# Performance work log

Measured on AMD Instinct MI355X. Metric: run time of the kernel, lower is better.

The kernel has to match this reference:

```python
import jax, jax.numpy as jnp
import numpy as np

B = 2097152
C = 10  # CIFAR-10 classes, hardcoded via `for j in range(10)` in the original


def setup_inputs() -> dict:
    key = jax.random.key(0)
    k1, k2, k3 = jax.random.split(key, 3)
    inp = jax.random.normal(k1, (B, C), dtype=jnp.float32)
    distance_matrix = jax.random.uniform(k2, (C, C), dtype=jnp.float32)
    target = jax.random.randint(k3, (B,), 0, C, dtype=jnp.int64)
    return {"input": inp, "distance_matrix": distance_matrix, "target": target}


def reference(input, distance_matrix, target):
    # distance_vector[i] = distance_matrix[target[i]]  -> [B, C]
    dv = distance_matrix[target]
    # distance_rank = argsort indices of each row (index of j-th smallest), as float
    r = jnp.argsort(dv, axis=1).astype(jnp.float32)  # [B, C]
    rt = jnp.take_along_axis(r, target[:, None], axis=1)  # [B, 1] rank entry at target position
    margins = jnp.maximum(0.0, 1.0 + r - rt)  # [B, C]
    mask = jnp.arange(C)[None, :] != target[:, None]  # exclude j == target[i]
    ranking_loss = jnp.sum(jnp.where(mask, margins, 0.0))
    # cross_entropy with mean reduction
    logp = jax.nn.log_softmax(input, axis=1)
    ce = -jnp.mean(jnp.take_along_axis(logp, target[:, None], axis=1))
    return ce + ranking_loss / input.shape[0]
```

## Files before the change

### kernel.cpp

```cpp
#include <hip/hip_runtime.h>

#define THREADS 256
#define BLOCKS  1024

__device__ __forceinline__ float row_loss10(
    float a0, float a1, float a2, float a3, float a4,
    float a5, float a6, float a7, float a8, float a9,
    int t, float sm)
{
    float m = fmaxf(fmaxf(fmaxf(a0, a1), fmaxf(a2, a3)),
                    fmaxf(fmaxf(fmaxf(a4, a5), fmaxf(a6, a7)), fmaxf(a8, a9)));
    float e0 = __expf(a0 - m), e1 = __expf(a1 - m);
    float e2 = __expf(a2 - m), e3 = __expf(a3 - m);
    float e4 = __expf(a4 - m), e5 = __expf(a5 - m);
    float e6 = __expf(a6 - m), e7 = __expf(a7 - m);
    float e8 = __expf(a8 - m), e9 = __expf(a9 - m);
    float s = ((e0 + e1) + (e2 + e3)) + (((e4 + e5) + (e6 + e7)) + (e8 + e9));
    float xt = a0;
    xt = (t == 1) ? a1 : xt;
    xt = (t == 2) ? a2 : xt;
    xt = (t == 3) ? a3 : xt;
    xt = (t == 4) ? a4 : xt;
    xt = (t == 5) ? a5 : xt;
    xt = (t == 6) ? a6 : xt;
    xt = (t == 7) ? a7 : xt;
    xt = (t == 8) ? a8 : xt;
    xt = (t == 9) ? a9 : xt;
    return m + __logf(s) - xt + sm;
}

__device__ __noinline__ float margin_for(const float* __restrict__ dm, int t) {
    float row[10];
    #pragma unroll
    for (int k = 0; k < 10; ++k) row[k] = dm[t * 10 + k];
    int rt = 0;
    #pragma unroll
    for (int k = 0; k < 10; ++k) {
        int cnt = 0;
        #pragma unroll
        for (int mi = 0; mi < 10; ++mi)
            cnt += (row[mi] < row[k]) || (row[mi] == row[k] && mi < k);
        if (cnt == t) rt = k;
    }
    float f = (float)(10 - rt);
    return 0.5f * f * (f + 1.0f) - 1.0f;
}

__global__ __launch_bounds__(THREADS, 4) void ranking_loss_kernel(
    const float* __restrict__ input,
    const float* __restrict__ dm,
    const int* __restrict__ target,
    float* __restrict__ partials,
    int B)
{
    __shared__ float4 stage[THREADS / 64][5 * 64];

    const int tid  = threadIdx.x;
    const int lane = tid & 63;
    const int wave = tid >> 6;

    float smval = 0.0f;
    if (lane < 10) {
        float row[10];
        #pragma unroll
        for (int k = 0; k < 10; ++k) row[k] = dm[lane * 10 + k];
        int rt = 0;
        #pragma unroll
        for (int k = 0; k < 10; ++k) {
            int cnt = 0;
            #pragma unroll
            for (int mi = 0; mi < 10; ++mi)
                cnt += (row[mi] < row[k]) || (row[mi] == row[k] && mi < k);
            if (cnt == lane) rt = k;
        }
        float f = (float)(10 - rt);
        smval = 0.5f * f * (f + 1.0f) - 1.0f;
    }

    const int nPairs  = B >> 1;
    const int gstride = gridDim.x * THREADS;
    float acc = 0.0f;

    float4* ws = stage[wave];
    int p0 = blockIdx.x * THREADS + wave * 64;

    float4 r0, r1, r2, r3, r4;
    int2 tt;
    bool have = (p0 + 64 <= nPairs);
    if (have) {
        const float4* g = (const float4*)input + (size_t)p0 * 5;
        r0 = g[0 * 64 + lane];
        r1 = g[1 * 64 + lane];
        r2 = g[2 * 64 + lane];
        r3 = g[3 * 64 + lane];
        r4 = g[4 * 64 + lane];
        tt = ((const int2*)target)[p0 + lane];
    }
    while (have) {
        ws[0 * 64 + lane] = r0;
        ws[1 * 64 + lane] = r1;
        ws[2 * 64 + lane] = r2;
        ws[3 * 64 + lane] = r3;
        ws[4 * 64 + lane] = r4;
        int2 ttc = tt;

        const int pn = p0 + gstride;
        const bool havenext = (pn + 64 <= nPairs);
        if (havenext) {
            const float4* g = (const float4*)input + (size_t)pn * 5;
            r0 = g[0 * 64 + lane];
            r1 = g[1 * 64 + lane];
            r2 = g[2 * 64 + lane];
            r3 = g[3 * 64 + lane];
            r4 = g[4 * 64 + lane];
            tt = ((const int2*)target)[pn + lane];
        }

        const float4* rp = &ws[(size_t)lane * 5];
        float4 q0 = rp[0], q1 = rp[1], q2 = rp[2], q3 = rp[3], q4 = rp[4];

        float sm0 = __shfl(smval, ttc.x, 64);
        float sm1 = __shfl(smval, ttc.y, 64);
        acc += row_loss10(q0.x, q0.y, q0.z, q0.w, q1.x, q1.y, q1.z, q1.w,
                          q2.x, q2.y, ttc.x, sm0);
        acc += row_loss10(q2.z, q2.w, q3.x, q3.y, q3.z, q3.w, q4.x, q4.y,
                          q4.z, q4.w, ttc.y, sm1);

        p0 = pn;
        have = havenext;
    }

    if (p0 < nPairs) {
        const int p = p0 + lane;
        if (p < nPairs) {
            const float* x = input + (size_t)p * 20;
            int t0 = target[2 * p], t1 = target[2 * p + 1];
            acc += row_loss10(x[0], x[1], x[2], x[3], x[4],
                              x[5], x[6], x[7], x[8], x[9], t0, margin_for(dm, t0));
            acc += row_loss10(x[10], x[11], x[12], x[13], x[14],
                              x[15], x[16], x[17], x[18], x[19], t1, margin_for(dm, t1));
        }
    }
    if ((B & 1) && blockIdx.x == 0 && tid == 0) {
        const float* x = input + (size_t)(B - 1) * 10;
        int t = target[B - 1];
        acc += row_loss10(x[0], x[1], x[2], x[3], x[4],
                          x[5], x[6], x[7], x[8], x[9], t, margin_for(dm, t));
    }

    #pragma unroll
    for (int off = 32; off > 0; off >>= 1)
        acc += __shfl_down(acc, off, 64);

    float* swsum = (float*)&stage[0][0];
    __syncthreads();
    if (lane == 0) swsum[wave] = acc;
    __syncthreads();
    if (tid == 0) {
        partials[blockIdx.x] = (swsum[0] + swsum[1]) + (swsum[2] + swsum[3]);
    }
}

__global__ __launch_bounds__(256) void reduce_kernel(
    const float* __restrict__ partials, float* __restrict__ out, float invB)
{
    __shared__ float sw[4];
    float a = 0.0f;
    #pragma unroll
    for (int k = 0; k < BLOCKS / 256; ++k)
        a += partials[k * 256 + threadIdx.x];
    #pragma unroll
    for (int off = 32; off > 0; off >>= 1)
        a += __shfl_down(a, off, 64);
    const int lane = threadIdx.x & 63;
    const int wave = threadIdx.x >> 6;
    if (lane == 0) sw[wave] = a;
    __syncthreads();
    if (threadIdx.x == 0)
        out[0] = ((sw[0] + sw[1]) + (sw[2] + sw[3])) * invB;
}

extern "C" void kernel_launch(void* const* d_in, const int* in_sizes, int n_in,
                              void* d_out, int out_size, void* d_ws, size_t ws_size,
                              hipStream_t stream) {
    const float* input  = (const float*)d_in[0];
    const float* dm     = (const float*)d_in[1];
    const int*   target = (const int*)d_in[2];
    float* out      = (float*)d_out;
    float* partials = (float*)d_ws;

    const int B = in_sizes[0] / 10;

    ranking_loss_kernel<<<BLOCKS, THREADS, 0, stream>>>(input, dm, target, partials, B);
    reduce_kernel<<<1, 256, 0, stream>>>(partials, out, 1.0f / (float)B);
}
```

Baseline: 131.3 us.

## Drop register prefetch, use nontemporal loads and double grid occupancy

Removes the software register double-buffering of the next tile, so each iteration loads, stages and computes in one step. Global loads become nontemporal, and the grid grows from 1024 to 2048 blocks while launch bounds rise to 8 waves per SIMD. The idea is to hide memory latency with more resident waves instead of per-thread prefetch registers. The risk is that without the explicit prefetch each wave stalls on its own loads, so the occupancy gain has to make up for that.

```diff
diff --git a/kernel.cpp b/kernel.cpp
--- a/kernel.cpp
+++ b/kernel.cpp
@@ -1,7 +1,10 @@
 #include <hip/hip_runtime.h>
 
 #define THREADS 256
-#define BLOCKS  1024
+#define BLOCKS  2048
+
+typedef float f4v __attribute__((ext_vector_type(4)));
+typedef int   i2v __attribute__((ext_vector_type(2)));
 
 __device__ __forceinline__ float row_loss10(
     float a0, float a1, float a2, float a3, float a4,
@@ -46,14 +49,14 @@
     return 0.5f * f * (f + 1.0f) - 1.0f;
 }
 
-__global__ __launch_bounds__(THREADS, 4) void ranking_loss_kernel(
+__global__ __launch_bounds__(THREADS, 8) void ranking_loss_kernel(
     const float* __restrict__ input,
     const float* __restrict__ dm,
     const int* __restrict__ target,
     float* __restrict__ partials,
     int B)
 {
-    __shared__ float4 stage[THREADS / 64][5 * 64];
+    __shared__ f4v stage[THREADS / 64][5 * 64];
 
     const int tid  = threadIdx.x;
     const int lane = tid & 63;
@@ -81,53 +84,33 @@
     const int gstride = gridDim.x * THREADS;
     float acc = 0.0f;
 
-    float4* ws = stage[wave];
+    f4v* ws = stage[wave];
     int p0 = blockIdx.x * THREADS + wave * 64;
 
-    float4 r0, r1, r2, r3, r4;
-    int2 tt;
-    bool have = (p0 + 64 <= nPairs);
-    if (have) {
-        const float4* g = (const float4*)input + (size_t)p0 * 5;
-        r0 = g[0 * 64 + lane];
-        r1 = g[1 * 64 + lane];
-        r2 = g[2 * 64 + lane];
-        r3 = g[3 * 64 + lane];
-        r4 = g[4 * 64 + lane];
-        tt = ((const int2*)target)[p0 + lane];
-    }
-    while (have) {
+    for (; p0 + 64 <= nPairs; p0 += gstride) {
+        const f4v* g = (const f4v*)input + (size_t)p0 * 5;
+        f4v r0 = __builtin_nontemporal_load(&g[0 * 64 + lane]);
+        f4v r1 = __builtin_nontemporal_load(&g[1 * 64 + lane]);
+        f4v r2 = __builtin_nontemporal_load(&g[2 * 64 + lane]);
+        f4v r3 = __builtin_nontemporal_load(&g[3 * 64 + lane]);
+        f4v r4 = __builtin_nontemporal_load(&g[4 * 64 + lane]);
+        i2v tt = __builtin_nontemporal_load(&((const i2v*)target)[p0 + lane]);
+
         ws[0 * 64 + lane] = r0;
         ws[1 * 64 + lane] = r1;
         ws[2 * 64 + lane] = r2;
         ws[3 * 64 + lane] = r3;
         ws[4 * 64 + lane] = r4;
-        int2 ttc = tt;
 
-        const int pn = p0 + gstride;
-        const bool havenext = (pn + 64 <= nPairs);
-        if (havenext) {
-            const float4* g = (const float4*)input + (size_t)pn * 5;
-            r0 = g[0 * 64 + lane];
-            r1 = g[1 * 64 + lane];
-            r2 = g[2 * 64 + lane];
-            r3 = g[3 * 64 + lane];
-            r4 = g[4 * 64 + lane];
-            tt = ((const int2*)target)[pn + lane];
-        }
+        const f4v* rp = &ws[(size_t)lane * 5];
+        f4v q0 = rp[0], q1 = rp[1], q2 = rp[2], q3 = rp[3], q4 = rp[4];
 
-        const float4* rp = &ws[(size_t)lane * 5];
-        float4 q0 = rp[0], q1 = rp[1], q2 = rp[2], q3 = rp[3], q4 = rp[4];
-
-        float sm0 = __shfl(smval, ttc.x, 64);
-        float sm1 = __shfl(smval, ttc.y, 64);
+        float sm0 = __shfl(smval, tt.x, 64);
+        float sm1 = __shfl(smval, tt.y, 64);
         acc += row_loss10(q0.x, q0.y, q0.z, q0.w, q1.x, q1.y, q1.z, q1.w,
-                          q2.x, q2.y, ttc.x, sm0);
+                          q2.x, q2.y, tt.x, sm0);
         acc += row_loss10(q2.z, q2.w, q3.x, q3.y, q3.z, q3.w, q4.x, q4.y,
-                          q4.z, q4.w, ttc.y, sm1);
-
-        p0 = pn;
-        have = havenext;
+                          q4.z, q4.w, tt.y, sm1);
     }
 
     if (p0 < nPairs) {
```

After: 124.7 us, median of 2. 5.0% less time.
